# Kernel optimization log

Hardware: AMD Instinct MI355X
Metric: run time of the kernel (lower is better)

Reference implementation:

```python
import jax, jax.numpy as jnp
import numpy as np

N = 4096          # nodes
E = 131072        # edges (avg degree 32)
D_IN = 128        # node_dim
H = 256           # hidden_dim
HEADS = 8
DH = H // HEADS


def setup_inputs() -> dict:
    key = jax.random.key(0)
    ks = jax.random.split(key, 24)
    w = lambda k, shape: (jax.random.normal(k, shape, dtype=jnp.float32) * 0.05)
    inp = {
        "x": jax.random.normal(ks[0], (N, D_IN), dtype=jnp.float32),
        "edge_index": jax.random.randint(ks[1], (2, E), 0, N, dtype=jnp.int32),
        # GCN conv weights (PyG GCNConv: out = aggr(norm * x @ W) + b)
        "W1": w(ks[2], (D_IN, H)), "b1": jnp.zeros((H,), jnp.float32),
        "W2": w(ks[3], (H, H)),    "b2": jnp.zeros((H,), jnp.float32),
        "W3": w(ks[4], (H, H)),    "b3": jnp.zeros((H,), jnp.float32),
        # nn.MultiheadAttention params (torch layout: y = x @ W.T + b)
        "in_w": w(ks[5], (3 * H, H)), "in_b": jnp.zeros((3 * H,), jnp.float32),
        "out_w": w(ks[6], (H, H)),    "out_b": jnp.zeros((H,), jnp.float32),
        # failure_predictor MLP: H -> H/2 -> 3
        "fp1_w": w(ks[7], (H // 2, H)), "fp1_b": jnp.zeros((H // 2,), jnp.float32),
        "fp2_w": w(ks[8], (3, H // 2)), "fp2_b": jnp.zeros((3,), jnp.float32),
        # pattern_detector MLP: H -> H/2 -> 10
        "pd1_w": w(ks[9], (H // 2, H)),  "pd1_b": jnp.zeros((H // 2,), jnp.float32),
        "pd2_w": w(ks[10], (10, H // 2)), "pd2_b": jnp.zeros((10,), jnp.float32),
    }
    return inp


def gcn_conv(x, src, dst, W, b):
    """PyG GCNConv with self-loops and symmetric normalization."""
    h = x @ W                                   # [N, H]
    deg = jnp.zeros((N,), x.dtype).at[dst].add(1.0) + 1.0   # +1 for self-loop
    dinv = jax.lax.rsqrt(deg)
    norm = dinv[src] * dinv[dst]                # [E]
    agg = jnp.zeros_like(h).at[dst].add(h[src] * norm[:, None])
    agg = agg + h * (1.0 / deg)[:, None]        # self-loop term: deg^-1/2 * deg^-1/2
    return agg + b


def mha(h, in_w, in_b, out_w, out_b):
    qkv = h @ in_w.T + in_b                     # [N, 3H]
    q, k, v = jnp.split(qkv, 3, axis=-1)
    q = q.reshape(N, HEADS, DH).transpose(1, 0, 2)   # [h, N, dh]
    k = k.reshape(N, HEADS, DH).transpose(1, 0, 2)
    v = v.reshape(N, HEADS, DH).transpose(1, 0, 2)
    scores = jnp.einsum("hnd,hmd->hnm", q, k) / np.sqrt(DH)
    attn = jax.nn.softmax(scores, axis=-1)
    o = jnp.einsum("hnm,hmd->hnd", attn, v)          # [h, N, dh]
    o = o.transpose(1, 0, 2).reshape(N, H)
    return o @ out_w.T + out_b


def reference(x, edge_index, W1, b1, W2, b2, W3, b3, in_w, in_b, out_w, out_b,
              fp1_w, fp1_b, fp2_w, fp2_b, pd1_w, pd1_b, pd2_w, pd2_b):
    src, dst = edge_index[0], edge_index[1]
    h = jax.nn.relu(gcn_conv(x, src, dst, W1, b1))   # dropout is identity in eval
    h = jax.nn.relu(gcn_conv(h, src, dst, W2, b2))
    h = gcn_conv(h, src, dst, W3, b3)
    h = h + mha(h, in_w, in_b, out_w, out_b)
    risk = jax.nn.softmax(jax.nn.relu(h @ fp1_w.T + fp1_b) @ fp2_w.T + fp2_b, axis=-1)
    patterns = jax.nn.sigmoid(jax.nn.relu(h @ pd1_w.T + pd1_b) @ pd2_w.T + pd2_b)
    return risk, patterns
```

## Files before the change

### kernel.cpp

```cpp
#include <hip/hip_runtime.h>
#include <math.h>

static constexpr int NNODE = 4096;
static constexpr int HDIM  = 256;
static constexpr int DIN   = 128;
static constexpr int HEADS = 8;
static constexpr int SPLIT = 4;

using short8 = __attribute__((ext_vector_type(8))) short;
using f32x4  = __attribute__((ext_vector_type(4))) float;

__device__ inline unsigned short bfr(float x) {
    union { float f; unsigned u; } v; v.f = x;
    unsigned r = v.u + 0x7FFFu + ((v.u >> 16) & 1u);
    return (unsigned short)(r >> 16);
}
__device__ inline float bf2f(unsigned short u) {
    union { unsigned u; float f; } v; v.u = (unsigned)u << 16; return v.f;
}
__device__ inline unsigned cvt_pk_bf16(float lo, float hi) {
    unsigned r;
    asm("v_cvt_pk_bf16_f32 %0, %1, %2" : "=v"(r) : "v"(lo), "v"(hi));
    return r;
}

static constexpr float QSCALE_LOG2 = 0.25503527f;

__global__ void k_deg(const int* __restrict__ ei, int* __restrict__ degi, int E) {
    int e = blockIdx.x * 256 + threadIdx.x;
    if (e < E) atomicAdd(&degi[ei[E + e]], 1);
}

__global__ __launch_bounds__(256) void k_scan_norm(const int* __restrict__ degi,
        int* __restrict__ off, int* __restrict__ cursor,
        float* __restrict__ dinv, float* __restrict__ invdeg) {
    __shared__ int partial[256];
    __shared__ int basesh[256];
    int t = threadIdx.x;
    int local[16];
    int s = 0;
    #pragma unroll
    for (int i = 0; i < 16; ++i) { local[i] = degi[t * 16 + i]; s += local[i]; }
    partial[t] = s;
    __syncthreads();
    if (t == 0) {
        int run = 0;
        for (int i = 0; i < 256; ++i) { basesh[i] = run; run += partial[i]; }
    }
    __syncthreads();
    int b = basesh[t];
    #pragma unroll
    for (int i = 0; i < 16; ++i) {
        int n = t * 16 + i;
        off[n] = b; cursor[n] = b; b += local[i];
        float d = (float)local[i] + 1.0f;
        dinv[n]   = rsqrtf(d);
        invdeg[n] = 1.0f / d;
    }
}

__global__ void k_fill(const int* __restrict__ ei, int* __restrict__ cursor,
                       int* __restrict__ csr, int E) {
    int e = blockIdx.x * 256 + threadIdx.x;
    if (e < E) {
        int d = ei[E + e];
        int p = atomicAdd(&cursor[d], 1);
        csr[p] = ei[e];
    }
}

__global__ __launch_bounds__(256) void k_prep(
        const float* __restrict__ W1, const float* __restrict__ W2,
        const float* __restrict__ W3, const float* __restrict__ in_w,
        const float* __restrict__ outw, const float* __restrict__ fp1w,
        const float* __restrict__ pd1w, const float* __restrict__ fp1b,
        const float* __restrict__ pd1b, const float* __restrict__ x,
        unsigned short* __restrict__ W1t, unsigned short* __restrict__ W2t,
        unsigned short* __restrict__ W3t, unsigned short* __restrict__ in_wb,
        unsigned short* __restrict__ outwb, unsigned short* __restrict__ wcatb,
        float* __restrict__ bcat, unsigned short* __restrict__ xb) {
    int idx = blockIdx.x * 256 + threadIdx.x;
    if (idx < 32768) {
        int c = idx >> 7, k = idx & 127;
        W1t[idx] = bfr(W1[(size_t)k * 256 + c]);
    } else if (idx < 98304) {
        int j = idx - 32768; int c = j >> 8, k = j & 255;
        W2t[j] = bfr(W2[(size_t)k * 256 + c]);
    } else if (idx < 163840) {
        int j = idx - 98304; int c = j >> 8, k = j & 255;
        W3t[j] = bfr(W3[(size_t)k * 256 + c]);
    } else if (idx < 360448) {
        int j = idx - 163840;
        in_wb[j] = bfr(in_w[j]);
    } else if (idx < 425984) {
        int j = idx - 360448;
        outwb[j] = bfr(outw[j]);
    } else if (idx < 491520) {
        int j = idx - 425984;
        int row = j >> 8, k = j & 255;
        wcatb[j] = bfr(row < 128 ? fp1w[(size_t)row * 256 + k]
                                 : pd1w[(size_t)(row - 128) * 256 + k]);
        if (j < 256) bcat[j] = (j < 128) ? fp1b[j] : pd1b[j - 128];
    } else if (idx < 557056) {
        int i = (idx - 491520) * 8;
        float4 a = *(const float4*)&x[i];
        float4 b = *(const float4*)&x[i + 4];
        short8 o;
        o[0]=(short)bfr(a.x); o[1]=(short)bfr(a.y); o[2]=(short)bfr(a.z); o[3]=(short)bfr(a.w);
        o[4]=(short)bfr(b.x); o[5]=(short)bfr(b.y); o[6]=(short)bfr(b.z); o[7]=(short)bfr(b.w);
        *(short8*)&xb[i] = o;
    }
}

template<int K, int EPI, bool BIAS, bool ADD>
__global__ __launch_bounds__(256) void k_bgemm(
        const unsigned short* __restrict__ A, const unsigned short* __restrict__ B,
        const float* __restrict__ bias, const float* __restrict__ addsrc,
        void* __restrict__ P0, void* __restrict__ P1, void* __restrict__ P2,
        int Nout) {
    const int lane = threadIdx.x & 63, wave = threadIdx.x >> 6;
    const int ql = lane & 15, g = lane >> 4;
    const int m0w = blockIdx.y * 64 + wave * 16;
    const int n0 = blockIdx.x * 32;
    const unsigned short* ap = A + (size_t)(m0w + ql) * K + g * 8;
    const unsigned short* bp = B + (size_t)(n0 + ql) * K + g * 8;

    f32x4 acc[2] = {{0,0,0,0},{0,0,0,0}};
    #pragma unroll
    for (int k0 = 0; k0 < K; k0 += 32) {
        short8 a = *(const short8*)(ap + k0);
        #pragma unroll
        for (int nt = 0; nt < 2; ++nt) {
            short8 b = *(const short8*)(bp + (size_t)nt * 16 * K + k0);
            acc[nt] = __builtin_amdgcn_mfma_f32_16x16x32_bf16(a, b, acc[nt], 0, 0, 0);
        }
    }
    #pragma unroll
    for (int nt = 0; nt < 2; ++nt) {
        const int col = n0 + nt * 16 + ql;
        const float bv = BIAS ? bias[col] : 0.f;
        if (EPI == 2) {
            const int sec = col >> 8, cc = col & 255;
            const int head = cc >> 5, dh = cc & 31;
            if (sec == 2) {
                unsigned short* dst = (unsigned short*)P2
                    + ((size_t)head * 32 + dh) * NNODE + m0w + g * 4;
                uint2 pk;
                pk.x = cvt_pk_bf16(acc[nt][0] + bv, acc[nt][1] + bv);
                pk.y = cvt_pk_bf16(acc[nt][2] + bv, acc[nt][3] + bv);
                *(uint2*)dst = pk;
            } else {
                unsigned short* dst = (unsigned short*)(sec == 0 ? P0 : P1);
                const float sc = (sec == 0) ? QSCALE_LOG2 : 1.0f;
                #pragma unroll
                for (int i = 0; i < 4; ++i) {
                    int row = m0w + g * 4 + i;
                    dst[((size_t)head * NNODE + row) * 32 + dh] = bfr((acc[nt][i] + bv) * sc);
                }
            }
        } else if (EPI == 1) {
            unsigned short* Cb = (unsigned short*)P0;
            #pragma unroll
            for (int i = 0; i < 4; ++i) {
                int row = m0w + g * 4 + i;
                float v = acc[nt][i] + bv;
                if (ADD) v += addsrc[(size_t)row * Nout + col];
                Cb[(size_t)row * Nout + col] = bfr(v);
            }
        } else {
            float* Cf = (float*)P0;
            #pragma unroll
            for (int i = 0; i < 4; ++i) {
                int row = m0w + g * 4 + i;
                float v = acc[nt][i] + bv;
                if (ADD) v += addsrc[(size_t)row * Nout + col];
                Cf[(size_t)row * Nout + col] = v;
            }
        }
    }
}

template<int MODE>
__global__ __launch_bounds__(256) void k_gather(const unsigned short* __restrict__ hW,
        const int* __restrict__ csr, const int* __restrict__ off,
        const int* __restrict__ degi, const float* __restrict__ dinv,
        const float* __restrict__ invdeg, const float* __restrict__ bias,
        float* __restrict__ aggf, unsigned short* __restrict__ aggb) {
    const int n = blockIdx.x;
    const int c = threadIdx.x;
    const int start = off[n];
    const int cnt = degi[n];
    __shared__ int   sidx[64];
    __shared__ float swht[64];
    float acc = 0.f;
    for (int k0 = 0; k0 < cnt; k0 += 64) {
        __syncthreads();
        if (c < 64 && k0 + c < cnt) {
            int s = csr[start + k0 + c];
            sidx[c] = s;
            swht[c] = dinv[s];
        }
        __syncthreads();
        int lim = min(64, cnt - k0);
        for (int k = 0; k < lim; ++k)
            acc += bf2f(hW[(size_t)sidx[k] * HDIM + c]) * swht[k];
    }
    float val = acc * dinv[n] + bf2f(hW[(size_t)n * HDIM + c]) * invdeg[n] + bias[c];
    if (MODE == 0) {
        aggb[(size_t)n * HDIM + c] = bfr(fmaxf(val, 0.f));
    } else {
        aggf[(size_t)n * HDIM + c] = val;
        aggb[(size_t)n * HDIM + c] = bfr(val);
    }
}

__global__ __launch_bounds__(256) void k_attn_mfma(const unsigned short* __restrict__ qh,
        const unsigned short* __restrict__ kh, const unsigned short* __restrict__ vt,
        unsigned short* __restrict__ po, float* __restrict__ pm, float* __restrict__ pl) {
    const int bid = blockIdx.x;
    const int hd = bid & 7;
    const int z  = (bid >> 3) & (SPLIT - 1);
    const int qb = bid >> 5;
    const int tid = threadIdx.x;
    const int wave = tid >> 6, lane = tid & 63;
    const int ql = lane & 15, g = lane >> 4;

    __shared__ unsigned short Vt[2][32 * 72];
    __shared__ unsigned short Plds[4][16 * 72];

    const unsigned short* khh = kh + (size_t)hd * NNODE * 32;
    const unsigned short* vtt = vt + (size_t)hd * 32 * NNODE;
    const int row = qb * 64 + wave * 16 + ql;
    short8 qf = *(const short8*)(qh + ((size_t)hd * NNODE + row) * 32 + g * 8);

    f32x4 oa0 = {0,0,0,0}, oa1 = {0,0,0,0};
    float m = -INFINITY, l = 0.f;

    const int sdh = tid >> 3, sch = (tid & 7) * 8;
    const unsigned short* vsrc = vtt + (size_t)sdh * NNODE + sch;
    const int TPS = NNODE / 64 / SPLIT;
    const int t0 = z * TPS;

    {
        short8 vv = *(const short8*)(vsrc + t0 * 64);
        *(short8*)&Vt[0][sdh * 72 + sch] = vv;
    }
    __syncthreads();
    int cur = 0;

    for (int kt = t0; kt < t0 + TPS; ++kt) {
        short8 vv;
        const bool pref = (kt + 1 < t0 + TPS);
        if (pref) vv = *(const short8*)(vsrc + (kt + 1) * 64);

        f32x4 st[4];
        #pragma unroll
        for (int t = 0; t < 4; ++t) {
            short8 kf = *(const short8*)(khh + (size_t)(kt * 64 + t * 16 + ql) * 32 + g * 8);
            st[t] = __builtin_amdgcn_mfma_f32_16x16x32_bf16(kf, qf, (f32x4){0,0,0,0}, 0, 0, 0);
        }

        float mloc = -INFINITY;
        #pragma unroll
        for (int t = 0; t < 4; ++t)
            mloc = fmaxf(mloc, fmaxf(fmaxf(st[t][0], st[t][1]), fmaxf(st[t][2], st[t][3])));
        mloc = fmaxf(mloc, __shfl_xor(mloc, 16));
        mloc = fmaxf(mloc, __shfl_xor(mloc, 32));

        if (!__all(mloc <= m + 8.f)) {
            float mnew = fmaxf(m, mloc);
            float corr = exp2f(m - mnew);
            l *= corr; oa0 *= corr; oa1 *= corr; m = mnew;
        }

        float ll = 0.f;
        unsigned pw[8];
        #pragma unroll
        for (int t = 0; t < 4; ++t) {
            float p0 = exp2f(st[t][0] - m);
            float p1 = exp2f(st[t][1] - m);
            float p2 = exp2f(st[t][2] - m);
            float p3 = exp2f(st[t][3] - m);
            ll += (p0 + p1) + (p2 + p3);
            pw[t * 2 + 0] = cvt_pk_bf16(p0, p1);
            pw[t * 2 + 1] = cvt_pk_bf16(p2, p3);
        }
        ll += __shfl_xor(ll, 16);
        ll += __shfl_xor(ll, 32);
        l += ll;

        #pragma unroll
        for (int t = 0; t < 4; ++t) {
            uint2 w2; w2.x = pw[t * 2 + 0]; w2.y = pw[t * 2 + 1];
            *(uint2*)&Plds[wave][ql * 72 + t * 16 + g * 4] = w2;
        }

        if (pref) *(short8*)&Vt[cur ^ 1][sdh * 72 + sch] = vv;

        #pragma unroll
        for (int c = 0; c < 2; ++c) {
            short8 pf = *(const short8*)&Plds[wave][ql * 72 + c * 32 + g * 8];
            short8 v0 = *(const short8*)&Vt[cur][ql * 72 + c * 32 + g * 8];
            short8 v1 = *(const short8*)&Vt[cur][(16 + ql) * 72 + c * 32 + g * 8];
            oa0 = __builtin_amdgcn_mfma_f32_16x16x32_bf16(v0, pf, oa0, 0, 0, 0);
            oa1 = __builtin_amdgcn_mfma_f32_16x16x32_bf16(v1, pf, oa1, 0, 0, 0);
        }
        __syncthreads();
        cur ^= 1;
    }

    const size_t pidx = ((size_t)hd * NNODE + row) * SPLIT + z;
    unsigned short* pp = po + pidx * 32;
    uint2 r0, r1;
    r0.x = cvt_pk_bf16(oa0[0], oa0[1]); r0.y = cvt_pk_bf16(oa0[2], oa0[3]);
    r1.x = cvt_pk_bf16(oa1[0], oa1[1]); r1.y = cvt_pk_bf16(oa1[2], oa1[3]);
    *(uint2*)&pp[g * 4]      = r0;
    *(uint2*)&pp[16 + g * 4] = r1;
    if (g == 0) { pm[pidx] = m; pl[pidx] = l; }
}

__global__ __launch_bounds__(256) void k_attn_merge(const unsigned short* __restrict__ po,
        const float* __restrict__ pm, const float* __restrict__ pl,
        unsigned short* __restrict__ ob) {
    int idx = blockIdx.x * 256 + threadIdx.x;
    int row = idx >> 8, c = idx & 255;
    int hd = c >> 5, dh = c & 31;
    size_t b4 = ((size_t)hd * NNODE + row) * SPLIT;
    float m0 = pm[b4+0], m1 = pm[b4+1], m2 = pm[b4+2], m3 = pm[b4+3];
    float M = fmaxf(fmaxf(m0, m1), fmaxf(m2, m3));
    float w0 = exp2f(m0 - M), w1 = exp2f(m1 - M);
    float w2 = exp2f(m2 - M), w3 = exp2f(m3 - M);
    float L = pl[b4]*w0 + pl[b4+1]*w1 + pl[b4+2]*w2 + pl[b4+3]*w3;
    float v = bf2f(po[(b4+0)*32 + dh])*w0 + bf2f(po[(b4+1)*32 + dh])*w1
            + bf2f(po[(b4+2)*32 + dh])*w2 + bf2f(po[(b4+3)*32 + dh])*w3;
    ob[idx] = bfr(v / L);
}

__global__ __launch_bounds__(256) void k_heads2(const float* __restrict__ th,
        const float* __restrict__ fp2w, const float* __restrict__ fp2b,
        const float* __restrict__ pd2w, const float* __restrict__ pd2b,
        float* __restrict__ out) {
    const int wave = threadIdx.x >> 6, lane = threadIdx.x & 63;
    const int n = blockIdx.x * 4 + wave;
    const int half = lane >> 5;
    const int li = lane & 31;
    float4 h4 = *(const float4*)&th[(size_t)n * HDIM + half * 128 + li * 4];
    h4.x = fmaxf(h4.x, 0.f); h4.y = fmaxf(h4.y, 0.f);
    h4.z = fmaxf(h4.z, 0.f); h4.w = fmaxf(h4.w, 0.f);
    float lf[3];
    float lp[10];
    #pragma unroll
    for (int j = 0; j < 10; ++j) {
        float partial = 0.f;
        if (half == 0) {
            if (j < 3) {
                float4 wv = *(const float4*)&fp2w[j * 128 + li * 4];
                partial = h4.x*wv.x + h4.y*wv.y + h4.z*wv.z + h4.w*wv.w;
            }
        } else {
            float4 wv = *(const float4*)&pd2w[j * 128 + li * 4];
            partial = h4.x*wv.x + h4.y*wv.y + h4.z*wv.z + h4.w*wv.w;
        }
        #pragma unroll
        for (int d = 1; d < 32; d <<= 1) partial += __shfl_xor(partial, d);
        if (j < 3) lf[j] = partial;
        lp[j] = partial;
    }
    if (lane == 0) {
        float l0 = lf[0] + fp2b[0], l1 = lf[1] + fp2b[1], l2 = lf[2] + fp2b[2];
        float mx = fmaxf(l0, fmaxf(l1, l2));
        float e0 = __expf(l0 - mx), e1 = __expf(l1 - mx), e2 = __expf(l2 - mx);
        float inv = 1.f / (e0 + e1 + e2);
        out[(size_t)n * 3 + 0] = e0 * inv;
        out[(size_t)n * 3 + 1] = e1 * inv;
        out[(size_t)n * 3 + 2] = e2 * inv;
    } else if (lane == 32) {
        #pragma unroll
        for (int j = 0; j < 10; ++j)
            out[(size_t)NNODE * 3 + (size_t)n * 10 + j] =
                1.f / (1.f + __expf(-(lp[j] + pd2b[j])));
    }
}

extern "C" void kernel_launch(void* const* d_in, const int* in_sizes, int n_in,
                              void* d_out, int out_size, void* d_ws, size_t ws_size,
                              hipStream_t stream) {
    const float* x    = (const float*)d_in[0];
    const int*   ei   = (const int*)  d_in[1];
    const float* W1   = (const float*)d_in[2];
    const float* b1   = (const float*)d_in[3];
    const float* W2   = (const float*)d_in[4];
    const float* b2   = (const float*)d_in[5];
    const float* W3   = (const float*)d_in[6];
    const float* b3   = (const float*)d_in[7];
    const float* in_w = (const float*)d_in[8];
    const float* in_b = (const float*)d_in[9];
    const float* outw = (const float*)d_in[10];
    const float* outb = (const float*)d_in[11];
    const float* fp1w = (const float*)d_in[12];
    const float* fp1b = (const float*)d_in[13];
    const float* fp2w = (const float*)d_in[14];
    const float* fp2b = (const float*)d_in[15];
    const float* pd1w = (const float*)d_in[16];
    const float* pd1b = (const float*)d_in[17];
    const float* pd2w = (const float*)d_in[18];
    const float* pd2b = (const float*)d_in[19];
    float* out = (float*)d_out;

    const int E = in_sizes[1] / 2;

    char* w = (char*)d_ws;
    auto alloc = [&](size_t bytes) {
        char* p = w; w += (bytes + 255) & ~(size_t)255; return p;
    };
    int*   degi   = (int*)alloc(NNODE * 4);
    int*   off    = (int*)alloc(NNODE * 4);
    int*   cursor = (int*)alloc(NNODE * 4);
    int*   csr    = (int*)alloc((size_t)E * 4);
    float* dinv   = (float*)alloc(NNODE * 4);
    float* invdeg = (float*)alloc(NNODE * 4);
    unsigned short* W1t   = (unsigned short*)alloc(256 * 128 * 2);
    unsigned short* W2t   = (unsigned short*)alloc(256 * 256 * 2);
    unsigned short* W3t   = (unsigned short*)alloc(256 * 256 * 2);
    unsigned short* in_wb = (unsigned short*)alloc(768 * 256 * 2);
    unsigned short* outwb = (unsigned short*)alloc(256 * 256 * 2);
    unsigned short* wcatb = (unsigned short*)alloc(256 * 256 * 2);
    float* bcat  = (float*)alloc(256 * 4);
    unsigned short* xb    = (unsigned short*)alloc((size_t)NNODE * DIN * 2);
    float* bufA  = (float*)alloc((size_t)NNODE * HDIM * 4);
    unsigned short* bufAb = (unsigned short*)alloc((size_t)NNODE * HDIM * 2);
    unsigned short* aggb1 = (unsigned short*)alloc((size_t)NNODE * HDIM * 2);
    unsigned short* aggb2 = (unsigned short*)alloc((size_t)NNODE * HDIM * 2);
    float* hf    = (float*)alloc((size_t)NNODE * HDIM * 4);
    unsigned short* hb    = (unsigned short*)alloc((size_t)NNODE * HDIM * 2);
    unsigned short* qh    = (unsigned short*)alloc((size_t)HEADS * NNODE * 32 * 2);
    unsigned short* kh    = (unsigned short*)alloc((size_t)HEADS * NNODE * 32 * 2);
    unsigned short* vt    = (unsigned short*)alloc((size_t)HEADS * 32 * NNODE * 2);
    unsigned short* po    = (unsigned short*)alloc((size_t)HEADS * NNODE * SPLIT * 32 * 2);
    float* pm    = (float*)alloc((size_t)HEADS * NNODE * SPLIT * 4);
    float* pl    = (float*)alloc((size_t)HEADS * NNODE * SPLIT * 4);
    unsigned short* ob    = (unsigned short*)alloc((size_t)NNODE * HDIM * 2);
    unsigned short* hfinb = (unsigned short*)alloc((size_t)NNODE * HDIM * 2);

    hipMemsetAsync(degi, 0, NNODE * sizeof(int), stream);
    k_deg<<<(E + 255) / 256, 256, 0, stream>>>(ei, degi, E);
    k_scan_norm<<<1, 256, 0, stream>>>(degi, off, cursor, dinv, invdeg);
    k_fill<<<(E + 255) / 256, 256, 0, stream>>>(ei, cursor, csr, E);
    k_prep<<<2176, 256, 0, stream>>>(W1, W2, W3, in_w, outw, fp1w, pd1w, fp1b, pd1b, x,
                                     W1t, W2t, W3t, in_wb, outwb, wcatb, bcat, xb);

    dim3 g256(HDIM / 32, NNODE / 64);
    dim3 g768(768 / 32, NNODE / 64);

    k_bgemm<DIN, 1, false, false><<<g256, 256, 0, stream>>>(xb, W1t, nullptr, nullptr, bufAb, nullptr, nullptr, HDIM);
    k_gather<0><<<NNODE, 256, 0, stream>>>(bufAb, csr, off, degi, dinv, invdeg, b1, nullptr, aggb1);
    k_bgemm<HDIM, 1, false, false><<<g256, 256, 0, stream>>>(aggb1, W2t, nullptr, nullptr, bufAb, nullptr, nullptr, HDIM);
    k_gather<0><<<NNODE, 256, 0, stream>>>(bufAb, csr, off, degi, dinv, invdeg, b2, nullptr, aggb2);
    k_bgemm<HDIM, 1, false, false><<<g256, 256, 0, stream>>>(aggb2, W3t, nullptr, nullptr, bufAb, nullptr, nullptr, HDIM);
    k_gather<1><<<NNODE, 256, 0, stream>>>(bufAb, csr, off, degi, dinv, invdeg, b3, hf, hb);

    k_bgemm<HDIM, 2, true, false><<<g768, 256, 0, stream>>>(hb, in_wb, in_b, nullptr, qh, kh, vt, 768);
    k_attn_mfma<<<HEADS * SPLIT * (NNODE / 64), 256, 0, stream>>>(qh, kh, vt, po, pm, pl);
    k_attn_merge<<<(NNODE * HDIM) / 256, 256, 0, stream>>>(po, pm, pl, ob);
    k_bgemm<HDIM, 1, true, true><<<g256, 256, 0, stream>>>(ob, outwb, outb, hf, hfinb, nullptr, nullptr, HDIM);

    k_bgemm<HDIM, 0, true, false><<<g256, 256, 0, stream>>>(hfinb, wcatb, bcat, nullptr, bufA, nullptr, nullptr, HDIM);
    k_heads2<<<NNODE / 4, 256, 0, stream>>>(bufA, fp2w, fp2b, pd2w, pd2b, out);
}
```

Baseline: 206.4 us.

## Process two query tiles per wave in attention to reuse K/V loads

Each attention wave now handles 32 query rows (two 16-row MFMA tiles) instead of 16, so every K fragment and V tile load feeds twice as many MFMAs, and the grid is halved. The change also replaces exp2f with raw v_exp_f32, adds s_setprio around the MFMA sections, and sets an occupancy hint in launch bounds. Separately, the serial single-thread prefix scan in k_scan_norm becomes a parallel Hillis-Steele scan. The trade-off is higher register pressure and fewer blocks (1024) in flight.

```diff
diff --git a/kernel.cpp b/kernel.cpp
--- a/kernel.cpp
+++ b/kernel.cpp
@@ -23,6 +23,11 @@
     asm("v_cvt_pk_bf16_f32 %0, %1, %2" : "=v"(r) : "v"(lo), "v"(hi));
     return r;
 }
+__device__ inline float ex2(float x) {
+    float r;
+    asm("v_exp_f32 %0, %1" : "=v"(r) : "v"(x));
+    return r;
+}
 
 static constexpr float QSCALE_LOG2 = 0.25503527f;
 
@@ -35,7 +40,6 @@
         int* __restrict__ off, int* __restrict__ cursor,
         float* __restrict__ dinv, float* __restrict__ invdeg) {
     __shared__ int partial[256];
-    __shared__ int basesh[256];
     int t = threadIdx.x;
     int local[16];
     int s = 0;
@@ -43,12 +47,14 @@
     for (int i = 0; i < 16; ++i) { local[i] = degi[t * 16 + i]; s += local[i]; }
     partial[t] = s;
     __syncthreads();
-    if (t == 0) {
-        int run = 0;
-        for (int i = 0; i < 256; ++i) { basesh[i] = run; run += partial[i]; }
-    }
-    __syncthreads();
-    int b = basesh[t];
+    #pragma unroll
+    for (int d = 1; d < 256; d <<= 1) {
+        int add = (t >= d) ? partial[t - d] : 0;
+        __syncthreads();
+        partial[t] += add;
+        __syncthreads();
+    }
+    int b = partial[t] - s;
     #pragma unroll
     for (int i = 0; i < 16; ++i) {
         int n = t * 16 + i;
@@ -214,7 +220,7 @@
     }
 }
 
-__global__ __launch_bounds__(256) void k_attn_mfma(const unsigned short* __restrict__ qh,
+__global__ __launch_bounds__(256, 4) void k_attn_mfma(const unsigned short* __restrict__ qh,
         const unsigned short* __restrict__ kh, const unsigned short* __restrict__ vt,
         unsigned short* __restrict__ po, float* __restrict__ pm, float* __restrict__ pl) {
     const int bid = blockIdx.x;
@@ -226,18 +232,22 @@
     const int ql = lane & 15, g = lane >> 4;
 
     __shared__ unsigned short Vt[2][32 * 72];
-    __shared__ unsigned short Plds[4][16 * 72];
+    __shared__ unsigned short Plds[4][32 * 72];
 
     const unsigned short* khh = kh + (size_t)hd * NNODE * 32;
     const unsigned short* vtt = vt + (size_t)hd * 32 * NNODE;
-    const int row = qb * 64 + wave * 16 + ql;
-    short8 qf = *(const short8*)(qh + ((size_t)hd * NNODE + row) * 32 + g * 8);
-
-    f32x4 oa0 = {0,0,0,0}, oa1 = {0,0,0,0};
-    float m = -INFINITY, l = 0.f;
+    const int row0 = qb * 128 + wave * 32 + ql;
+    const int row1 = row0 + 16;
+    short8 qf0 = *(const short8*)(qh + ((size_t)hd * NNODE + row0) * 32 + g * 8);
+    short8 qf1 = *(const short8*)(qh + ((size_t)hd * NNODE + row1) * 32 + g * 8);
+
+    f32x4 oa00 = {0,0,0,0}, oa01 = {0,0,0,0};
+    f32x4 oa10 = {0,0,0,0}, oa11 = {0,0,0,0};
+    float m0 = -INFINITY, l0 = 0.f, m1 = -INFINITY, l1 = 0.f;
 
     const int sdh = tid >> 3, sch = (tid & 7) * 8;
     const unsigned short* vsrc = vtt + (size_t)sdh * NNODE + sch;
+    const unsigned short* kbase = khh + (size_t)ql * 32 + g * 8;
     const int TPS = NNODE / 64 / SPLIT;
     const int t0 = z * TPS;
 
@@ -253,70 +263,104 @@
         const bool pref = (kt + 1 < t0 + TPS);
         if (pref) vv = *(const short8*)(vsrc + (kt + 1) * 64);
 
-        f32x4 st[4];
+        f32x4 st0[4], st1[4];
+        __builtin_amdgcn_s_setprio(1);
         #pragma unroll
         for (int t = 0; t < 4; ++t) {
-            short8 kf = *(const short8*)(khh + (size_t)(kt * 64 + t * 16 + ql) * 32 + g * 8);
-            st[t] = __builtin_amdgcn_mfma_f32_16x16x32_bf16(kf, qf, (f32x4){0,0,0,0}, 0, 0, 0);
-        }
-
-        float mloc = -INFINITY;
-        #pragma unroll
-        for (int t = 0; t < 4; ++t)
-            mloc = fmaxf(mloc, fmaxf(fmaxf(st[t][0], st[t][1]), fmaxf(st[t][2], st[t][3])));
-        mloc = fmaxf(mloc, __shfl_xor(mloc, 16));
-        mloc = fmaxf(mloc, __shfl_xor(mloc, 32));
-
-        if (!__all(mloc <= m + 8.f)) {
-            float mnew = fmaxf(m, mloc);
-            float corr = exp2f(m - mnew);
-            l *= corr; oa0 *= corr; oa1 *= corr; m = mnew;
-        }
-
-        float ll = 0.f;
-        unsigned pw[8];
-        #pragma unroll
-        for (int t = 0; t < 4; ++t) {
-            float p0 = exp2f(st[t][0] - m);
-            float p1 = exp2f(st[t][1] - m);
-            float p2 = exp2f(st[t][2] - m);
-            float p3 = exp2f(st[t][3] - m);
-            ll += (p0 + p1) + (p2 + p3);
-            pw[t * 2 + 0] = cvt_pk_bf16(p0, p1);
-            pw[t * 2 + 1] = cvt_pk_bf16(p2, p3);
-        }
-        ll += __shfl_xor(ll, 16);
-        ll += __shfl_xor(ll, 32);
-        l += ll;
-
-        #pragma unroll
-        for (int t = 0; t < 4; ++t) {
-            uint2 w2; w2.x = pw[t * 2 + 0]; w2.y = pw[t * 2 + 1];
-            *(uint2*)&Plds[wave][ql * 72 + t * 16 + g * 4] = w2;
+            short8 kf = *(const short8*)(kbase + ((size_t)kt * 64 + t * 16) * 32);
+            st0[t] = __builtin_amdgcn_mfma_f32_16x16x32_bf16(kf, qf0, (f32x4){0,0,0,0}, 0, 0, 0);
+            st1[t] = __builtin_amdgcn_mfma_f32_16x16x32_bf16(kf, qf1, (f32x4){0,0,0,0}, 0, 0, 0);
+        }
+        __builtin_amdgcn_s_setprio(0);
+
+        {
+            float mloc = -INFINITY;
+            #pragma unroll
+            for (int t = 0; t < 4; ++t)
+                mloc = fmaxf(mloc, fmaxf(fmaxf(st0[t][0], st0[t][1]), fmaxf(st0[t][2], st0[t][3])));
+            mloc = fmaxf(mloc, __shfl_xor(mloc, 16));
+            mloc = fmaxf(mloc, __shfl_xor(mloc, 32));
+            if (!__all(mloc <= m0 + 8.f)) {
+                float mnew = fmaxf(m0, mloc);
+                float corr = ex2(m0 - mnew);
+                l0 *= corr; oa00 *= corr; oa01 *= corr; m0 = mnew;
+            }
+            float ll = 0.f;
+            #pragma unroll
+            for (int t = 0; t < 4; ++t) {
+                float p0 = ex2(st0[t][0] - m0);
+                float p1 = ex2(st0[t][1] - m0);
+                float p2 = ex2(st0[t][2] - m0);
+                float p3 = ex2(st0[t][3] - m0);
+                ll += (p0 + p1) + (p2 + p3);
+                uint2 w2; w2.x = cvt_pk_bf16(p0, p1); w2.y = cvt_pk_bf16(p2, p3);
+                *(uint2*)&Plds[wave][ql * 72 + t * 16 + g * 4] = w2;
+            }
+            ll += __shfl_xor(ll, 16);
+            ll += __shfl_xor(ll, 32);
+            l0 += ll;
+        }
+        {
+            float mloc = -INFINITY;
+            #pragma unroll
+            for (int t = 0; t < 4; ++t)
+                mloc = fmaxf(mloc, fmaxf(fmaxf(st1[t][0], st1[t][1]), fmaxf(st1[t][2], st1[t][3])));
+            mloc = fmaxf(mloc, __shfl_xor(mloc, 16));
+            mloc = fmaxf(mloc, __shfl_xor(mloc, 32));
+            if (!__all(mloc <= m1 + 8.f)) {
+                float mnew = fmaxf(m1, mloc);
+                float corr = ex2(m1 - mnew);
+                l1 *= corr; oa10 *= corr; oa11 *= corr; m1 = mnew;
+            }
+            float ll = 0.f;
+            #pragma unroll
+            for (int t = 0; t < 4; ++t) {
+                float p0 = ex2(st1[t][0] - m1);
+                float p1 = ex2(st1[t][1] - m1);
+                float p2 = ex2(st1[t][2] - m1);
+                float p3 = ex2(st1[t][3] - m1);
+                ll += (p0 + p1) + (p2 + p3);
+                uint2 w2; w2.x = cvt_pk_bf16(p0, p1); w2.y = cvt_pk_bf16(p2, p3);
+                *(uint2*)&Plds[wave][(16 + ql) * 72 + t * 16 + g * 4] = w2;
+            }
+            ll += __shfl_xor(ll, 16);
+            ll += __shfl_xor(ll, 32);
+            l1 += ll;
         }
 
         if (pref) *(short8*)&Vt[cur ^ 1][sdh * 72 + sch] = vv;
 
+        __builtin_amdgcn_s_setprio(1);
         #pragma unroll
         for (int c = 0; c < 2; ++c) {
-            short8 pf = *(const short8*)&Plds[wave][ql * 72 + c * 32 + g * 8];
-            short8 v0 = *(const short8*)&Vt[cur][ql * 72 + c * 32 + g * 8];
-            short8 v1 = *(const short8*)&Vt[cur][(16 + ql) * 72 + c * 32 + g * 8];
-            oa0 = __builtin_amdgcn_mfma_f32_16x16x32_bf16(v0, pf, oa0, 0, 0, 0);
-            oa1 = __builtin_amdgcn_mfma_f32_16x16x32_bf16(v1, pf, oa1, 0, 0, 0);
-        }
+            short8 v0  = *(const short8*)&Vt[cur][ql * 72 + c * 32 + g * 8];
+            short8 v1  = *(const short8*)&Vt[cur][(16 + ql) * 72 + c * 32 + g * 8];
+            short8 pf0 = *(const short8*)&Plds[wave][ql * 72 + c * 32 + g * 8];
+            short8 pf1 = *(const short8*)&Plds[wave][(16 + ql) * 72 + c * 32 + g * 8];
+            oa00 = __builtin_amdgcn_mfma_f32_16x16x32_bf16(v0, pf0, oa00, 0, 0, 0);
+            oa01 = __builtin_amdgcn_mfma_f32_16x16x32_bf16(v1, pf0, oa01, 0, 0, 0);
+            oa10 = __builtin_amdgcn_mfma_f32_16x16x32_bf16(v0, pf1, oa10, 0, 0, 0);
+            oa11 = __builtin_amdgcn_mfma_f32_16x16x32_bf16(v1, pf1, oa11, 0, 0, 0);
+        }
+        __builtin_amdgcn_s_setprio(0);
         __syncthreads();
         cur ^= 1;
     }
 
-    const size_t pidx = ((size_t)hd * NNODE + row) * SPLIT + z;
-    unsigned short* pp = po + pidx * 32;
-    uint2 r0, r1;
-    r0.x = cvt_pk_bf16(oa0[0], oa0[1]); r0.y = cvt_pk_bf16(oa0[2], oa0[3]);
-    r1.x = cvt_pk_bf16(oa1[0], oa1[1]); r1.y = cvt_pk_bf16(oa1[2], oa1[3]);
-    *(uint2*)&pp[g * 4]      = r0;
-    *(uint2*)&pp[16 + g * 4] = r1;
-    if (g == 0) { pm[pidx] = m; pl[pidx] = l; }
+    const size_t pidx0 = ((size_t)hd * NNODE + row0) * SPLIT + z;
+    const size_t pidx1 = ((size_t)hd * NNODE + row1) * SPLIT + z;
+    unsigned short* pp0 = po + pidx0 * 32;
+    unsigned short* pp1 = po + pidx1 * 32;
+    uint2 r;
+    r.x = cvt_pk_bf16(oa00[0], oa00[1]); r.y = cvt_pk_bf16(oa00[2], oa00[3]);
+    *(uint2*)&pp0[g * 4] = r;
+    r.x = cvt_pk_bf16(oa01[0], oa01[1]); r.y = cvt_pk_bf16(oa01[2], oa01[3]);
+    *(uint2*)&pp0[16 + g * 4] = r;
+    r.x = cvt_pk_bf16(oa10[0], oa10[1]); r.y = cvt_pk_bf16(oa10[2], oa10[3]);
+    *(uint2*)&pp1[g * 4] = r;
+    r.x = cvt_pk_bf16(oa11[0], oa11[1]); r.y = cvt_pk_bf16(oa11[2], oa11[3]);
+    *(uint2*)&pp1[16 + g * 4] = r;
+    if (g == 0) { pm[pidx0] = m0; pl[pidx0] = l0; pm[pidx1] = m1; pl[pidx1] = l1; }
 }
 
 __global__ __launch_bounds__(256) void k_attn_merge(const unsigned short* __restrict__ po,
@@ -328,8 +372,8 @@
     size_t b4 = ((size_t)hd * NNODE + row) * SPLIT;
     float m0 = pm[b4+0], m1 = pm[b4+1], m2 = pm[b4+2], m3 = pm[b4+3];
     float M = fmaxf(fmaxf(m0, m1), fmaxf(m2, m3));
-    float w0 = exp2f(m0 - M), w1 = exp2f(m1 - M);
-    float w2 = exp2f(m2 - M), w3 = exp2f(m3 - M);
+    float w0 = ex2(m0 - M), w1 = ex2(m1 - M);
+    float w2 = ex2(m2 - M), w3 = ex2(m3 - M);
     float L = pl[b4]*w0 + pl[b4+1]*w1 + pl[b4+2]*w2 + pl[b4+3]*w3;
     float v = bf2f(po[(b4+0)*32 + dh])*w0 + bf2f(po[(b4+1)*32 + dh])*w1
             + bf2f(po[(b4+2)*32 + dh])*w2 + bf2f(po[(b4+3)*32 + dh])*w3;
@@ -460,7 +504,7 @@
     k_gather<1><<<NNODE, 256, 0, stream>>>(bufAb, csr, off, degi, dinv, invdeg, b3, hf, hb);
 
     k_bgemm<HDIM, 2, true, false><<<g768, 256, 0, stream>>>(hb, in_wb, in_b, nullptr, qh, kh, vt, 768);
-    k_attn_mfma<<<HEADS * SPLIT * (NNODE / 64), 256, 0, stream>>>(qh, kh, vt, po, pm, pl);
+    k_attn_mfma<<<HEADS * SPLIT * (NNODE / 128), 256, 0, stream>>>(qh, kh, vt, po, pm, pl);
     k_attn_merge<<<(NNODE * HDIM) / 256, 256, 0, stream>>>(po, pm, pl, ob);
     k_bgemm<HDIM, 1, true, true><<<g256, 256, 0, stream>>>(ob, outwb, outb, hf, hfinb, nullptr, nullptr, HDIM);
 
```

Result: faster. 183.7 us (-11.0%).
